# Performance work log

Hardware: AMD Instinct MI355X
Metric: run time of the kernel (lower is better)

The kernel has to match this reference:

```python
import jax, jax.numpy as jnp
import numpy as np
from jax.ops import segment_sum, segment_max

N_NODES = 100000
N_EDGES = 1600000
IN, HID, OUT = 256, 64, 40
NEG_SLOPE = 0.2  # DGL GATConv default


def setup_inputs() -> dict:
    key = jax.random.key(0)
    ks = jax.random.split(key, 12)
    feat = jax.random.normal(ks[0], (N_NODES, IN), dtype=jnp.float32)
    src = jax.random.randint(ks[1], (N_EDGES,), 0, N_NODES)
    dst = jax.random.randint(ks[2], (N_EDGES,), 0, N_NODES)
    def xavier(k, shape):
        fan = sum(shape)
        return jax.random.normal(k, shape, dtype=jnp.float32) * jnp.sqrt(2.0 / fan)
    return {
        "feat": feat, "src": src, "dst": dst,
        "W1": xavier(ks[3], (IN, HID)),  "b1": jnp.zeros((HID,), jnp.float32),
        "al1": xavier(ks[4], (HID,)),    "ar1": xavier(ks[5], (HID,)),
        "W2": xavier(ks[6], (HID, OUT)), "b2": jnp.zeros((OUT,), jnp.float32),
        "al2": xavier(ks[7], (OUT,)),    "ar2": xavier(ks[8], (OUT,)),
    }


def gat_layer(x, W, b, attn_l, attn_r, src, dst, n):
    # z: [N, F_out] projected features
    z = x @ W
    el = z @ attn_l          # [N] source attention logits
    er = z @ attn_r          # [N] destination attention logits
    e = jax.nn.leaky_relu(el[src] + er[dst], NEG_SLOPE)  # [E]
    # segment (per-destination) softmax over incoming edges
    m = segment_max(e, dst, num_segments=n)              # [N]
    w = jnp.exp(e - m[dst])                              # [E]
    s = segment_sum(w, dst, num_segments=n)              # [N]
    alpha = w / s[dst]                                   # [E]
    # scatter-add aggregation of alpha * z[src]
    out = segment_sum(alpha[:, None] * z[src], dst, num_segments=n)
    return out + b


def reference(feat, src, dst, W1, b1, al1, ar1, W2, b2, al2, ar2):
    n = feat.shape[0]
    h = gat_layer(feat, W1, b1, al1, ar1, src, dst, n)
    h = jax.nn.relu(h)  # dropout is identity in eval mode
    h = gat_layer(h, W2, b2, al2, ar2, src, dst, n)
    return jax.nn.log_softmax(h, axis=-1)  # [N, out_size]
```

## Files before the change

### kernel.cpp

```cpp
#include <hip/hip_runtime.h>
#include <math.h>

constexpr int NN   = 100000;
constexpr int NE   = 1600000;
constexpr int FIN  = 256;
constexpr int HID  = 64;
constexpr int FOUT = 40;
constexpr float SLOPE = 0.2f;
constexpr int NB    = (NN + 255) / 256;
constexpr int NBUCK = NB;
constexpr int TILE_A = 2048;
constexpr int NWG_A = (NE + TILE_A - 1) / TILE_A;
constexpr int AK = 264;

typedef short  short8  __attribute__((ext_vector_type(8)));
typedef float  floatx4 __attribute__((ext_vector_type(4)));

__device__ inline unsigned short f2bf(float x) {
    union { float f; unsigned int u; } c; c.f = x;
    unsigned int u = c.u;
    return (unsigned short)((u + 0x7FFF + ((u >> 16) & 1)) >> 16);
}

__device__ inline float readlane_f(float v, int l) {
    return __int_as_float(__builtin_amdgcn_readlane(__float_as_int(v), l));
}

__global__ __launch_bounds__(256) void w1t_kernel(
    const float* __restrict__ W1, unsigned short* __restrict__ W1T)
{
    int idx = blockIdx.x * 256 + threadIdx.x;
    if (idx < FIN * HID) {
        int k = idx >> 6, n = idx & 63;
        W1T[n * FIN + k] = f2bf(W1[idx]);
    }
}

__global__ __launch_bounds__(256) void gemm1_kernel(
    const float* __restrict__ feat, const unsigned short* __restrict__ W1T,
    const float* __restrict__ al, const float* __restrict__ ar,
    const int* __restrict__ dst, int* __restrict__ bcnt,
    _Float16* __restrict__ z, float* __restrict__ el, float* __restrict__ er)
{
    __shared__ unsigned short sBT[64 * AK];
    __shared__ int hist[NBUCK];
    const int t = threadIdx.x;
    const int ntile = blockIdx.x * 64;

    for (int i = t; i < NBUCK; i += 256) hist[i] = 0;
    #pragma unroll
    for (int i = 0; i < 8; ++i) {
        int g = t + 256 * i;
        int row = g >> 5, c8 = g & 31;
        *(uint4*)&sBT[row * AK + 8 * c8] = *(const uint4*)&W1T[row * FIN + 8 * c8];
    }
    __syncthreads();

    {
        int base = (blockIdx.x * 256 + t) * 4;
        if (base < NE) {
            const int4 d4 = *(const int4*)&dst[base];
            atomicAdd(&hist[d4.x >> 8], 1); atomicAdd(&hist[d4.y >> 8], 1);
            atomicAdd(&hist[d4.z >> 8], 1); atomicAdd(&hist[d4.w >> 8], 1);
        }
    }
    __syncthreads();
    for (int i = t; i < NBUCK; i += 256) {
        int hv = hist[i];
        if (hv) atomicAdd(&bcnt[i], hv);
    }

    const int w  = t >> 6;
    const int l  = t & 63;
    const int lr = l & 15;
    const int q  = l >> 4;
    const int m0 = 16 * w;

    int n = ntile + m0 + lr; if (n >= NN) n = NN - 1;
    const float* __restrict__ arow = feat + (size_t)n * FIN;

    floatx4 acc[4];
    #pragma unroll
    for (int tile = 0; tile < 4; ++tile) acc[tile] = 0.f;

    #pragma unroll
    for (int kc = 0; kc < 8; ++kc) {
        const int koff = kc * 32 + 8 * q;
        const float4 fa = *(const float4*)(arow + koff);
        const float4 fb = *(const float4*)(arow + koff + 4);
        short8 av;
        av[0] = (short)f2bf(fa.x); av[1] = (short)f2bf(fa.y);
        av[2] = (short)f2bf(fa.z); av[3] = (short)f2bf(fa.w);
        av[4] = (short)f2bf(fb.x); av[5] = (short)f2bf(fb.y);
        av[6] = (short)f2bf(fb.z); av[7] = (short)f2bf(fb.w);
        #pragma unroll
        for (int tile = 0; tile < 4; ++tile) {
            const short8 bv = *(const short8*)(sBT + (16 * tile + lr) * AK + koff);
            acc[tile] = __builtin_amdgcn_mfma_f32_16x16x32_bf16(av, bv, acc[tile], 0, 0, 0);
        }
    }

    float aln[4], arn[4];
    #pragma unroll
    for (int tile = 0; tile < 4; ++tile) {
        aln[tile] = al[16 * tile + lr];
        arn[tile] = ar[16 * tile + lr];
    }
    #pragma unroll
    for (int r = 0; r < 4; ++r) {
        int mg = ntile + m0 + 4 * q + r;
        float pl = 0.f, pr = 0.f;
        #pragma unroll
        for (int tile = 0; tile < 4; ++tile) {
            float zv = acc[tile][r];
            pl += zv * aln[tile]; pr += zv * arn[tile];
        }
        #pragma unroll
        for (int off = 8; off >= 1; off >>= 1) {
            pl += __shfl_xor(pl, off);
            pr += __shfl_xor(pr, off);
        }
        if (mg < NN) {
            #pragma unroll
            for (int tile = 0; tile < 4; ++tile)
                z[(size_t)mg * HID + 16 * tile + lr] = (_Float16)acc[tile][r];
            if (lr == 0) { el[mg] = pl; er[mg] = pr; }
        }
    }
}

__global__ __launch_bounds__(256) void gemm2_kernel(
    const float* __restrict__ h, const float* __restrict__ W2,
    const float* __restrict__ al, const float* __restrict__ ar,
    _Float16* __restrict__ z2, float* __restrict__ el, float* __restrict__ er)
{
    __shared__ float sh[4][64];
    const int w = threadIdx.x >> 6, lane = threadIdx.x & 63;
    const int n = blockIdx.x * 4 + w;
    sh[w][lane] = h[(size_t)n * HID + lane];
    __syncthreads();
    float acc = 0.f;
    if (lane < FOUT) {
        #pragma unroll 8
        for (int k = 0; k < 64; ++k) acc += sh[w][k] * W2[k * FOUT + lane];
    }
    float pl = (lane < FOUT) ? acc * al[lane] : 0.f;
    float pr = (lane < FOUT) ? acc * ar[lane] : 0.f;
    #pragma unroll
    for (int off = 32; off >= 1; off >>= 1) { pl += __shfl_xor(pl, off); pr += __shfl_xor(pr, off); }
    if (lane == 0) { el[n] = pl; er[n] = pr; }
    if (lane < FOUT) z2[(size_t)n * FOUT + lane] = (_Float16)acc;
}

__global__ __launch_bounds__(512) void scan_top_kernel(
    const int* __restrict__ bcnt, int* __restrict__ bofs, int* __restrict__ gcur)
{
    __shared__ int tmp[512];
    int t = threadIdx.x;
    int v = (t < NB) ? bcnt[t] : 0;
    tmp[t] = v; __syncthreads();
    for (int off = 1; off < 512; off <<= 1) {
        int x = (t >= off) ? tmp[t - off] : 0;
        __syncthreads();
        tmp[t] += x;
        __syncthreads();
    }
    int excl = tmp[t] - v;
    if (t < NB) { bofs[t] = excl; gcur[t] = excl; }
    if (t == NB - 1) bofs[NB] = excl + v;
}

__global__ __launch_bounds__(256) void partitionA_kernel(
    const int* __restrict__ src, const int* __restrict__ dst,
    int* __restrict__ gcur, int* __restrict__ ebuck)
{
    __shared__ int hist[NBUCK];
    __shared__ int lcur[NBUCK];
    const int t = threadIdx.x;
    const int e0 = blockIdx.x * TILE_A;
    const int e1 = (e0 + TILE_A < NE) ? e0 + TILE_A : NE;

    for (int i = t; i < NBUCK; i += 256) hist[i] = 0;
    __syncthreads();
    for (int e = e0 + t; e < e1; e += 256)
        atomicAdd(&hist[dst[e] >> 8], 1);
    __syncthreads();
    for (int i = t; i < NBUCK; i += 256) {
        int hv = hist[i];
        lcur[i] = hv ? atomicAdd(&gcur[i], hv) : 0;
    }
    __syncthreads();
    for (int e = e0 + t; e < e1; e += 256) {
        int d = dst[e], s = src[e];
        int p = atomicAdd(&lcur[d >> 8], 1);
        ebuck[p] = (s << 8) | (d & 255);
    }
}

__global__ __launch_bounds__(256) void partitionB_kernel(
    const int* __restrict__ bofs, const int* __restrict__ ebuck,
    int* __restrict__ row_ptr, int* __restrict__ esrc)
{
    __shared__ int sdeg[256];
    __shared__ int sscan[256];
    const int b = blockIdx.x;
    const int n0 = b << 8;
    const int t = threadIdx.x;
    const int r0 = bofs[b], r1 = bofs[b + 1];

    sdeg[t] = 0;
    __syncthreads();
    for (int e = r0 + t; e < r1; e += 256)
        atomicAdd(&sdeg[ebuck[e] & 255], 1);
    __syncthreads();

    int v = sdeg[t];
    sscan[t] = v;
    __syncthreads();
    for (int off = 1; off < 256; off <<= 1) {
        int x = (t >= off) ? sscan[t - off] : 0;
        __syncthreads();
        sscan[t] += x;
        __syncthreads();
    }
    int excl = sscan[t] - v;
    if (n0 + t < NN) row_ptr[n0 + t] = r0 + excl;
    if (b == NBUCK - 1 && t == 0) row_ptr[NN] = NE;

    sdeg[t] = r0 + excl;
    __syncthreads();
    for (int e = r0 + t; e < r1; e += 256) {
        int pk = ebuck[e];
        int p = atomicAdd(&sdeg[pk & 255], 1);
        esrc[p] = pk >> 8;
    }
}

template<int F, bool FINAL_LAYER>
__global__ __launch_bounds__(256) void gat_gather_kernel(
    const int* __restrict__ row_ptr, const int* __restrict__ esrc,
    const float* __restrict__ el, const float* __restrict__ er,
    const _Float16* __restrict__ z, const float* __restrict__ bias,
    float* __restrict__ out)
{
    const int w = threadIdx.x >> 6, lane = threadIdx.x & 63;
    const int d = blockIdx.x * 4 + w;
    const int r0 = row_ptr[d], r1 = row_ptr[d + 1];
    const int cnt = r1 - r0;
    const float erd = er[d];

    float accv = 0.f;
    float s = 0.f;

    if (cnt <= 64) {
        int sn = 0; float v = -INFINITY;
        if (lane < cnt) {
            sn = esrc[r0 + lane];
            v = el[sn] + erd;
            v = (v >= 0.f) ? v : SLOPE * v;
        }
        float m = v;
        #pragma unroll
        for (int off = 32; off >= 1; off >>= 1) m = fmaxf(m, __shfl_xor(m, off));
        float wv = (lane < cnt) ? __expf(v - m) : 0.f;
        s = wv;
        #pragma unroll
        for (int off = 32; off >= 1; off >>= 1) s += __shfl_xor(s, off);
        if (lane < F) {
            int j = 0;
            for (; j + 8 <= cnt; j += 8) {
                float a0 = 0.f, a1 = 0.f;
                #pragma unroll
                for (int qq = 0; qq < 8; qq += 2) {
                    float w0 = readlane_f(wv, j + qq);
                    int   s0 = __builtin_amdgcn_readlane(sn, j + qq);
                    float w1 = readlane_f(wv, j + qq + 1);
                    int   s1 = __builtin_amdgcn_readlane(sn, j + qq + 1);
                    a0 += w0 * (float)z[(size_t)s0 * F + lane];
                    a1 += w1 * (float)z[(size_t)s1 * F + lane];
                }
                accv += a0 + a1;
            }
            for (; j < cnt; ++j) {
                float w0 = readlane_f(wv, j);
                int   s0 = __builtin_amdgcn_readlane(sn, j);
                accv += w0 * (float)z[(size_t)s0 * F + lane];
            }
        }
    } else {
        float m = -INFINITY;
        for (int e = r0 + lane; e < r1; e += 64) {
            float v = el[esrc[e]] + erd;
            v = (v >= 0.f) ? v : SLOPE * v;
            m = fmaxf(m, v);
        }
        #pragma unroll
        for (int off = 32; off >= 1; off >>= 1) m = fmaxf(m, __shfl_xor(m, off));
        for (int base = r0; base < r1; base += 64) {
            int e = base + lane;
            float wv = 0.f; int sn = 0;
            if (e < r1) {
                sn = esrc[e];
                float v = el[sn] + erd;
                v = (v >= 0.f) ? v : SLOPE * v;
                wv = __expf(v - m);
            }
            s += wv;
            int c = r1 - base; if (c > 64) c = 64;
            if (lane < F) {
                int j = 0;
                for (; j + 4 <= c; j += 4) {
                    float a0 = 0.f, a1 = 0.f;
                    #pragma unroll
                    for (int qq = 0; qq < 4; qq += 2) {
                        float w0 = readlane_f(wv, j + qq);
                        int   s0 = __builtin_amdgcn_readlane(sn, j + qq);
                        float w1 = readlane_f(wv, j + qq + 1);
                        int   s1 = __builtin_amdgcn_readlane(sn, j + qq + 1);
                        a0 += w0 * (float)z[(size_t)s0 * F + lane];
                        a1 += w1 * (float)z[(size_t)s1 * F + lane];
                    }
                    accv += a0 + a1;
                }
                for (; j < c; ++j) {
                    float w0 = readlane_f(wv, j);
                    int   s0 = __builtin_amdgcn_readlane(sn, j);
                    accv += w0 * (float)z[(size_t)s0 * F + lane];
                }
            }
        }
        #pragma unroll
        for (int off = 32; off >= 1; off >>= 1) s += __shfl_xor(s, off);
    }

    float res = (cnt > 0) ? (accv / s) : 0.f;

    if (!FINAL_LAYER) {
        if (lane < F) {
            float v = res + bias[lane];
            out[(size_t)d * F + lane] = (v > 0.f) ? v : 0.f;
        }
    } else {
        float v = (lane < F) ? res + bias[lane] : -INFINITY;
        float mx = v;
        #pragma unroll
        for (int off = 32; off >= 1; off >>= 1) mx = fmaxf(mx, __shfl_xor(mx, off));
        float ex = (lane < F) ? __expf(v - mx) : 0.f;
        float sm = ex;
        #pragma unroll
        for (int off = 32; off >= 1; off >>= 1) sm += __shfl_xor(sm, off);
        if (lane < F) out[(size_t)d * F + lane] = v - mx - __logf(sm);
    }
}

extern "C" void kernel_launch(void* const* d_in, const int* in_sizes, int n_in,
                              void* d_out, int out_size, void* d_ws, size_t ws_size,
                              hipStream_t stream) {
    const float* feat = (const float*)d_in[0];
    const int*   src  = (const int*)d_in[1];
    const int*   dst  = (const int*)d_in[2];
    const float* W1   = (const float*)d_in[3];
    const float* b1   = (const float*)d_in[4];
    const float* al1  = (const float*)d_in[5];
    const float* ar1  = (const float*)d_in[6];
    const float* W2   = (const float*)d_in[7];
    const float* b2   = (const float*)d_in[8];
    const float* al2  = (const float*)d_in[9];
    const float* ar2  = (const float*)d_in[10];
    float* out = (float*)d_out;

    float* ws    = (float*)d_ws;
    _Float16* z1 = (_Float16*)ws;
    float* h     = ws + (size_t)NN * HID / 2 + 64;
    float* el1   = h + (size_t)NN * HID;
    float* er1   = el1 + NN;
    float* el2   = er1 + NN;
    float* er2   = el2 + NN;
    int*   bcnt  = (int*)(er2 + NN);
    int*   bofs  = bcnt + NB;
    int*   gcur  = bofs + NB + 1;
    int*   rowp  = gcur + NBUCK;
    int*   esrc  = rowp + NN + 1;
    unsigned short* w1t = (unsigned short*)(esrc + NE);
    int*   ebuck = (int*)h;
    _Float16* z2 = z1;

    hipMemsetAsync(bcnt, 0, NB * sizeof(int), stream);

    w1t_kernel<<<(FIN * HID + 255) / 256, 256, 0, stream>>>(W1, w1t);
    gemm1_kernel<<<(NN + 63) / 64, 256, 0, stream>>>(feat, w1t, al1, ar1, dst, bcnt, z1, el1, er1);

    scan_top_kernel<<<1, 512, 0, stream>>>(bcnt, bofs, gcur);
    partitionA_kernel<<<NWG_A, 256, 0, stream>>>(src, dst, gcur, ebuck);
    partitionB_kernel<<<NBUCK, 256, 0, stream>>>(bofs, ebuck, rowp, esrc);

    gat_gather_kernel<HID, false><<<NN / 4, 256, 0, stream>>>(rowp, esrc, el1, er1, z1, b1, h);

    gemm2_kernel<<<NN / 4, 256, 0, stream>>>(h, W2, al2, ar2, z2, el2, er2);
    gat_gather_kernel<FOUT, true><<<NN / 4, 256, 0, stream>>>(rowp, esrc, el2, er2, z2, b2, out);
}
```

Before: 451.4 us.

## Fuse layer-2 projection into layer-1 gather and widen partition blocks

The second-layer GEMM (h·W2 plus attention logits) now runs inside the first-layer gather epilogue, so the fp32 hidden tensor h is never written to or read back from global memory, and one kernel launch goes away. Each gather block now stages the whole 64x40 W2 matrix in shared memory, which adds per-block load traffic and LDS use and may reduce occupancy. The partition kernels move from 256 to 1024 threads per block. The workspace is re-laid out so ebuck and z2 get their own buffers instead of aliasing h and z1.

```diff
diff --git a/kernel.cpp b/kernel.cpp
--- a/kernel.cpp
+++ b/kernel.cpp
@@ -129,29 +129,6 @@
     }
 }
 
-__global__ __launch_bounds__(256) void gemm2_kernel(
-    const float* __restrict__ h, const float* __restrict__ W2,
-    const float* __restrict__ al, const float* __restrict__ ar,
-    _Float16* __restrict__ z2, float* __restrict__ el, float* __restrict__ er)
-{
-    __shared__ float sh[4][64];
-    const int w = threadIdx.x >> 6, lane = threadIdx.x & 63;
-    const int n = blockIdx.x * 4 + w;
-    sh[w][lane] = h[(size_t)n * HID + lane];
-    __syncthreads();
-    float acc = 0.f;
-    if (lane < FOUT) {
-        #pragma unroll 8
-        for (int k = 0; k < 64; ++k) acc += sh[w][k] * W2[k * FOUT + lane];
-    }
-    float pl = (lane < FOUT) ? acc * al[lane] : 0.f;
-    float pr = (lane < FOUT) ? acc * ar[lane] : 0.f;
-    #pragma unroll
-    for (int off = 32; off >= 1; off >>= 1) { pl += __shfl_xor(pl, off); pr += __shfl_xor(pr, off); }
-    if (lane == 0) { el[n] = pl; er[n] = pr; }
-    if (lane < FOUT) z2[(size_t)n * FOUT + lane] = (_Float16)acc;
-}
-
 __global__ __launch_bounds__(512) void scan_top_kernel(
     const int* __restrict__ bcnt, int* __restrict__ bofs, int* __restrict__ gcur)
 {
@@ -170,7 +147,7 @@
     if (t == NB - 1) bofs[NB] = excl + v;
 }
 
-__global__ __launch_bounds__(256) void partitionA_kernel(
+__global__ __launch_bounds__(1024) void partitionA_kernel(
     const int* __restrict__ src, const int* __restrict__ dst,
     int* __restrict__ gcur, int* __restrict__ ebuck)
 {
@@ -180,58 +157,61 @@
     const int e0 = blockIdx.x * TILE_A;
     const int e1 = (e0 + TILE_A < NE) ? e0 + TILE_A : NE;
 
-    for (int i = t; i < NBUCK; i += 256) hist[i] = 0;
-    __syncthreads();
-    for (int e = e0 + t; e < e1; e += 256)
+    for (int i = t; i < NBUCK; i += 1024) hist[i] = 0;
+    __syncthreads();
+    for (int e = e0 + t; e < e1; e += 1024)
         atomicAdd(&hist[dst[e] >> 8], 1);
     __syncthreads();
-    for (int i = t; i < NBUCK; i += 256) {
+    for (int i = t; i < NBUCK; i += 1024) {
         int hv = hist[i];
         lcur[i] = hv ? atomicAdd(&gcur[i], hv) : 0;
     }
     __syncthreads();
-    for (int e = e0 + t; e < e1; e += 256) {
+    for (int e = e0 + t; e < e1; e += 1024) {
         int d = dst[e], s = src[e];
         int p = atomicAdd(&lcur[d >> 8], 1);
         ebuck[p] = (s << 8) | (d & 255);
     }
 }
 
-__global__ __launch_bounds__(256) void partitionB_kernel(
+__global__ __launch_bounds__(1024) void partitionB_kernel(
     const int* __restrict__ bofs, const int* __restrict__ ebuck,
     int* __restrict__ row_ptr, int* __restrict__ esrc)
 {
     __shared__ int sdeg[256];
     __shared__ int sscan[256];
+    __shared__ int scur[256];
     const int b = blockIdx.x;
     const int n0 = b << 8;
     const int t = threadIdx.x;
     const int r0 = bofs[b], r1 = bofs[b + 1];
 
-    sdeg[t] = 0;
-    __syncthreads();
-    for (int e = r0 + t; e < r1; e += 256)
+    if (t < 256) sdeg[t] = 0;
+    __syncthreads();
+    for (int e = r0 + t; e < r1; e += 1024)
         atomicAdd(&sdeg[ebuck[e] & 255], 1);
     __syncthreads();
 
-    int v = sdeg[t];
-    sscan[t] = v;
+    if (t < 256) sscan[t] = sdeg[t];
     __syncthreads();
     for (int off = 1; off < 256; off <<= 1) {
-        int x = (t >= off) ? sscan[t - off] : 0;
+        int x = 0;
+        if (t < 256 && t >= off) x = sscan[t - off];
         __syncthreads();
-        sscan[t] += x;
+        if (t < 256) sscan[t] += x;
         __syncthreads();
     }
-    int excl = sscan[t] - v;
-    if (n0 + t < NN) row_ptr[n0 + t] = r0 + excl;
+    if (t < 256) {
+        int excl = sscan[t] - sdeg[t];
+        if (n0 + t < NN) row_ptr[n0 + t] = r0 + excl;
+        scur[t] = r0 + excl;
+    }
     if (b == NBUCK - 1 && t == 0) row_ptr[NN] = NE;
-
-    sdeg[t] = r0 + excl;
-    __syncthreads();
-    for (int e = r0 + t; e < r1; e += 256) {
+    __syncthreads();
+
+    for (int e = r0 + t; e < r1; e += 1024) {
         int pk = ebuck[e];
-        int p = atomicAdd(&sdeg[pk & 255], 1);
+        int p = atomicAdd(&scur[pk & 255], 1);
         esrc[p] = pk >> 8;
     }
 }
@@ -241,13 +221,23 @@
     const int* __restrict__ row_ptr, const int* __restrict__ esrc,
     const float* __restrict__ el, const float* __restrict__ er,
     const _Float16* __restrict__ z, const float* __restrict__ bias,
+    const float* __restrict__ W2, const float* __restrict__ al2,
+    const float* __restrict__ ar2,
+    _Float16* __restrict__ z2, float* __restrict__ el2, float* __restrict__ er2,
     float* __restrict__ out)
 {
+    __shared__ float sW2[HID * FOUT];
+    __shared__ float sh[4][HID];
     const int w = threadIdx.x >> 6, lane = threadIdx.x & 63;
     const int d = blockIdx.x * 4 + w;
     const int r0 = row_ptr[d], r1 = row_ptr[d + 1];
     const int cnt = r1 - r0;
     const float erd = er[d];
+
+    if (!FINAL_LAYER) {
+        for (int i = threadIdx.x; i < HID * FOUT; i += 256) sW2[i] = W2[i];
+        __syncthreads();
+    }
 
     float accv = 0.f;
     float s = 0.f;
@@ -336,10 +326,22 @@
     float res = (cnt > 0) ? (accv / s) : 0.f;
 
     if (!FINAL_LAYER) {
-        if (lane < F) {
-            float v = res + bias[lane];
-            out[(size_t)d * F + lane] = (v > 0.f) ? v : 0.f;
-        }
+        float hval = res + bias[lane];
+        hval = (hval > 0.f) ? hval : 0.f;
+        sh[w][lane] = hval;
+        float acc2 = 0.f;
+        if (lane < FOUT) {
+            #pragma unroll 8
+            for (int k = 0; k < HID; ++k) acc2 += sh[w][k] * sW2[k * FOUT + lane];
+        }
+        float pl = (lane < FOUT) ? acc2 * al2[lane] : 0.f;
+        float pr = (lane < FOUT) ? acc2 * ar2[lane] : 0.f;
+        #pragma unroll
+        for (int off = 32; off >= 1; off >>= 1) {
+            pl += __shfl_xor(pl, off); pr += __shfl_xor(pr, off);
+        }
+        if (lane == 0) { el2[d] = pl; er2[d] = pr; }
+        if (lane < FOUT) z2[(size_t)d * FOUT + lane] = (_Float16)acc2;
     } else {
         float v = (lane < F) ? res + bias[lane] : -INFINITY;
         float mx = v;
@@ -369,21 +371,20 @@
     const float* ar2  = (const float*)d_in[10];
     float* out = (float*)d_out;
 
-    float* ws    = (float*)d_ws;
-    _Float16* z1 = (_Float16*)ws;
-    float* h     = ws + (size_t)NN * HID / 2 + 64;
-    float* el1   = h + (size_t)NN * HID;
-    float* er1   = el1 + NN;
-    float* el2   = er1 + NN;
-    float* er2   = el2 + NN;
-    int*   bcnt  = (int*)(er2 + NN);
-    int*   bofs  = bcnt + NB;
-    int*   gcur  = bofs + NB + 1;
-    int*   rowp  = gcur + NBUCK;
-    int*   esrc  = rowp + NN + 1;
-    unsigned short* w1t = (unsigned short*)(esrc + NE);
-    int*   ebuck = (int*)h;
-    _Float16* z2 = z1;
+    char* p = (char*)d_ws;
+    _Float16* z1 = (_Float16*)p;  p += (size_t)NN * HID * 2;
+    _Float16* z2 = (_Float16*)p;  p += (size_t)NN * FOUT * 2;
+    float* el1   = (float*)p;     p += (size_t)NN * 4;
+    float* er1   = (float*)p;     p += (size_t)NN * 4;
+    float* el2   = (float*)p;     p += (size_t)NN * 4;
+    float* er2   = (float*)p;     p += (size_t)NN * 4;
+    int*   bcnt  = (int*)p;       p += NB * 4;
+    int*   bofs  = (int*)p;       p += (NB + 1) * 4;
+    int*   gcur  = (int*)p;       p += NBUCK * 4;
+    int*   rowp  = (int*)p;       p += (NN + 1) * 4;
+    int*   esrc  = (int*)p;       p += (size_t)NE * 4;
+    int*   ebuck = (int*)p;       p += (size_t)NE * 4;
+    unsigned short* w1t = (unsigned short*)p;
 
     hipMemsetAsync(bcnt, 0, NB * sizeof(int), stream);
 
@@ -391,11 +392,13 @@
     gemm1_kernel<<<(NN + 63) / 64, 256, 0, stream>>>(feat, w1t, al1, ar1, dst, bcnt, z1, el1, er1);
 
     scan_top_kernel<<<1, 512, 0, stream>>>(bcnt, bofs, gcur);
-    partitionA_kernel<<<NWG_A, 256, 0, stream>>>(src, dst, gcur, ebuck);
-    partitionB_kernel<<<NBUCK, 256, 0, stream>>>(bofs, ebuck, rowp, esrc);
-
-    gat_gather_kernel<HID, false><<<NN / 4, 256, 0, stream>>>(rowp, esrc, el1, er1, z1, b1, h);
-
-    gemm2_kernel<<<NN / 4, 256, 0, stream>>>(h, W2, al2, ar2, z2, el2, er2);
-    gat_gather_kernel<FOUT, true><<<NN / 4, 256, 0, stream>>>(rowp, esrc, el2, er2, z2, b2, out);
-}
+    partitionA_kernel<<<NWG_A, 1024, 0, stream>>>(src, dst, gcur, ebuck);
+    partitionB_kernel<<<NBUCK, 1024, 0, stream>>>(bofs, ebuck, rowp, esrc);
+
+    gat_gather_kernel<HID, false><<<NN / 4, 256, 0, stream>>>(
+        rowp, esrc, el1, er1, z1, b1, W2, al2, ar2, z2, el2, er2, nullptr);
+
+    gat_gather_kernel<FOUT, true><<<NN / 4, 256, 0, stream>>>(
+        rowp, esrc, el2, er2, z2, b2, nullptr, nullptr, nullptr,
+        nullptr, nullptr, nullptr, out);
+}
```

Measured after the change: 414.0 us. 8.3% less time.
